# Performance work log

Hardware: AMD Instinct MI355X
Metric: run time of the kernel (lower is better)

Reference implementation:

```python
import jax, jax.numpy as jnp
import numpy as np

S = 64   # feature-map height/width = sqrt(qvk_dim)
M = 2    # memory_block_size


def _block_divide(t):
    # (b, c, S*S) -> (b, c, (S/M)**2, M*M), matching
    # Rearrange('b c (h m1) (w m2) -> b c (h w) (m1 m2)')
    b, c, _ = t.shape
    h = S // M
    t = t.reshape(b, c, h, M, h, M)
    t = jnp.transpose(t, (0, 1, 2, 4, 3, 5))
    return t.reshape(b, c, h * h, M * M)


def setup_inputs() -> dict:
    key = jax.random.key(0)
    k1, k2, k3, k4 = jax.random.split(key, 4)
    B, C, F = 64, 64, S * S
    x = jax.random.normal(k1, (B, C, F), dtype=jnp.float32)
    scale = 1.0 / np.sqrt(F)
    Wq = jax.random.normal(k2, (F, F), dtype=jnp.float32) * scale
    Wk = jax.random.normal(k3, (F, F), dtype=jnp.float32) * scale
    Wv = jax.random.normal(k4, (F, F), dtype=jnp.float32) * scale
    return {"x": x, "Wq": Wq, "Wk": Wk, "Wv": Wv}


def reference(x, Wq, Wk, Wv):
    # Linear(in, out, bias=False): y = x @ W.T, W: (out, in)
    q = _block_divide(jnp.einsum('bcf,qf->bcq', x, Wq))  # (b,c,n,g)
    k = _block_divide(jnp.einsum('bcf,qf->bcq', x, Wk))  # (b,c,n,p)
    v = _block_divide(jnp.einsum('bcf,qf->bcq', x, Wv))  # (b,c,n,p)
    # score[b,c,n,g,p] = q[b,c,n,g] * k[b,c,n,p]; softmax over p (dim=4)
    score = q[..., :, None] * k[..., None, :]             # (b,c,n,g,p)
    att = jax.nn.softmax(score, axis=-1)
    # matmul(att (g,p), v (p,1)) -> (g,1), then flatten blocks
    out = jnp.einsum('bcngp,bcnp->bcng', att, v)          # (b,c,n,g)
    b, c, n, g = out.shape
    return out.reshape(b, c, n * g)
```

## Files before the change

kernel.cpp:

```cpp
#include <hip/hip_runtime.h>

#define F        4096
#define NE       ((size_t)F * F)

typedef __attribute__((ext_vector_type(8))) short bf16x8;
typedef __attribute__((ext_vector_type(4))) float f32x4;

typedef const void __attribute__((address_space(1)))* gas1p;
typedef void __attribute__((address_space(3)))*       as3p;

__device__ __forceinline__ void gload16(const void* g, void* l) {
    __builtin_amdgcn_global_load_lds((gas1p)g, (as3p)l, 16, 0, 0);
}

__device__ __forceinline__ unsigned short f2bf(float f) {
    union { float f; unsigned int u; } c; c.f = f;
    unsigned int u = c.u;
    u += 0x7fffu + ((u >> 16) & 1u);
    return (unsigned short)(u >> 16);
}
__device__ __forceinline__ float bf2f(unsigned short u) {
    union { unsigned int u; float f; } c; c.u = ((unsigned int)u) << 16;
    return c.f;
}

__global__ void cvt_all(const float* __restrict__ s0, const float* __restrict__ s1,
                        const float* __restrict__ s2, const float* __restrict__ s3,
                        unsigned short* __restrict__ d0, unsigned short* __restrict__ d1,
                        unsigned short* __restrict__ d2, unsigned short* __restrict__ d3,
                        int n4) {
    const float* src = (blockIdx.y == 0) ? s0 : (blockIdx.y == 1) ? s1
                      : (blockIdx.y == 2) ? s2 : s3;
    unsigned short* dst = (blockIdx.y == 0) ? d0 : (blockIdx.y == 1) ? d1
                         : (blockIdx.y == 2) ? d2 : d3;
    int idx    = blockIdx.x * blockDim.x + threadIdx.x;
    int stride = gridDim.x * blockDim.x;
    const float4* in4 = (const float4*)src;
    ushort4* out4 = (ushort4*)dst;
    for (int i = idx; i < n4; i += stride) {
        float4 v = in4[i];
        ushort4 o;
        o.x = f2bf(v.x); o.y = f2bf(v.y); o.z = f2bf(v.z); o.w = f2bf(v.w);
        out4[i] = o;
    }
}

__device__ __forceinline__ int qo_map(int o) {
    int nblk = o >> 2, g = o & 3;
    return (nblk >> 5) * 128 + (g >> 1) * 64 + (nblk & 31) * 2 + (g & 1);
}

#define MFMA16(a, b, c) __builtin_amdgcn_mfma_f32_16x16x32_bf16(a, b, c, 0, 0, 0)

#define GBM 256
#define GBN 256
#define GBK 32
#define NKT (F / GBK)
#define ELPS (GBM * GBK)

__launch_bounds__(512, 1)
__global__ void gemm_qkv(const unsigned short* __restrict__ Xb,
                         const unsigned short* __restrict__ Qw,
                         const unsigned short* __restrict__ Kw,
                         const unsigned short* __restrict__ Vw,
                         unsigned short* __restrict__ qkv) {
    __shared__ __align__(16) unsigned short Als[4][GBM][GBK];
    __shared__ __align__(16) unsigned short Bls[4][GBN][GBK];

    const int tid  = threadIdx.x;
    const int lane = tid & 63;
    const int wid  = tid >> 6;
    const int wm   = wid >> 2;
    const int wn   = wid & 3;

    const int bid = blockIdx.x;
    const int swz = (bid & 7) * 96 + (bid >> 3);
    const int mt  = swz & 15;
    const int nt  = swz >> 4;
    const int bm  = mt * GBM;
    const int bnG = nt * GBN;
    const int mat = bnG >> 12;
    const int bn  = bnG & 4095;
    const unsigned short* __restrict__ Wsel = (mat == 0) ? Qw : (mat == 1) ? Kw : Vw;

    const int sr_row = tid >> 2;
    const int sr_chn = (tid & 3) ^ ((tid >> 3) & 3);
    const unsigned short* aSrc0 = Xb + (size_t)(bm + sr_row) * F + sr_chn * 8;
    const unsigned short* aSrc1 = aSrc0 + (size_t)128 * F;
    const unsigned short* bSrc0 = Wsel + (size_t)qo_map(bn + sr_row) * F + sr_chn * 8;
    const unsigned short* bSrc1 = Wsel + (size_t)qo_map(bn + 128 + sr_row) * F + sr_chn * 8;

#define STAGE_A(s, tt) do {                                                     \
        gload16(aSrc0 + (size_t)(tt) * GBK, (void*)&Als[s][wid * 16][0]);       \
        gload16(aSrc1 + (size_t)(tt) * GBK, (void*)&Als[s][128 + wid * 16][0]); \
    } while (0)
#define STAGE_B(s, tt) do {                                                     \
        gload16(bSrc0 + (size_t)(tt) * GBK, (void*)&Bls[s][wid * 16][0]);       \
        gload16(bSrc1 + (size_t)(tt) * GBK, (void*)&Bls[s][128 + wid * 16][0]); \
    } while (0)

    const int fr  = lane & 15;
    const int fq  = lane >> 4;
    const int fq2 = fq ^ ((fr >> 1) & 3);
    const unsigned short* aRd = &Als[0][wm * 128 + fr][fq2 * 8];
    const unsigned short* bRd = &Bls[0][wn * 64 + fr][fq2 * 8];

    f32x4 acc[8][4];
#pragma unroll
    for (int m = 0; m < 8; ++m)
#pragma unroll
        for (int n = 0; n < 4; ++n)
            acc[m][n] = (f32x4){0.f, 0.f, 0.f, 0.f};

    STAGE_A(0, 0); STAGE_B(0, 0);
    STAGE_A(1, 1); STAGE_B(1, 1);
    STAGE_A(2, 2); STAGE_B(2, 2);
    asm volatile("s_waitcnt vmcnt(4)" ::: "memory");
    __builtin_amdgcn_s_barrier();
    __builtin_amdgcn_sched_barrier(0);

    bf16x8 af[8], bf[4];
#pragma unroll
    for (int m = 0; m < 8; ++m) af[m] = *(const bf16x8*)(aRd + m * 512);
#pragma unroll
    for (int n = 0; n < 4; ++n) bf[n] = *(const bf16x8*)(bRd + n * 512);

#pragma unroll 4
    for (int t = 0; t < NKT; ++t) {
        const int sn = (t + 1) & 3;
        const int ss = (t + 3) & 3;
        const int tt = (t + 3) & (NKT - 1);
        const unsigned short* aN = aRd + sn * ELPS;
        const unsigned short* bN = bRd + sn * ELPS;

        __builtin_amdgcn_s_setprio(1);
#pragma unroll
        for (int m = 0; m < 8; ++m) {
#pragma unroll
            for (int n = 0; n < 4; ++n)
                acc[m][n] = MFMA16(af[m], bf[n], acc[m][n]);
            af[m] = *(const bf16x8*)(aN + m * 512);
        }
#pragma unroll
        for (int n = 0; n < 4; ++n)
            bf[n] = *(const bf16x8*)(bN + n * 512);
        __builtin_amdgcn_s_setprio(0);

        STAGE_A(ss, tt);
        STAGE_B(ss, tt);
        __builtin_amdgcn_sched_barrier(0);
        asm volatile("s_waitcnt vmcnt(4)" ::: "memory");
        __builtin_amdgcn_sched_barrier(0);
        __builtin_amdgcn_s_barrier();
    }

    unsigned short* outB = qkv + (size_t)mat * NE;
#pragma unroll
    for (int m = 0; m < 8; ++m) {
#pragma unroll
        for (int n = 0; n < 4; ++n) {
#pragma unroll
            for (int r = 0; r < 4; ++r) {
                int row = bm + wm * 128 + m * 16 + fq * 4 + r;
                int col = bn + wn * 64 + n * 16 + fr;
                outB[(size_t)row * F + col] = f2bf(acc[m][n][r]);
            }
        }
    }
#undef STAGE_A
#undef STAGE_B
}

__global__ void attn_ep(const unsigned short* __restrict__ qkv,
                        float* __restrict__ out) {
    const size_t NB = NE / 4;
    const ushort4* q4 = (const ushort4*)qkv;
    const ushort4* k4 = q4 + NB;
    const ushort4* v4 = k4 + NB;
    float4* o4 = (float4*)out;
    size_t i      = (size_t)blockIdx.x * blockDim.x + threadIdx.x;
    size_t stride = (size_t)gridDim.x * blockDim.x;
    for (; i < NB; i += stride) {
        ushort4 qu = q4[i], ku = k4[i], vu = v4[i];
        float q0 = bf2f(qu.x), q1 = bf2f(qu.y), q2 = bf2f(qu.z), q3 = bf2f(qu.w);
        float k0 = bf2f(ku.x), k1 = bf2f(ku.y), k2 = bf2f(ku.z), k3 = bf2f(ku.w);
        float v0 = bf2f(vu.x), v1 = bf2f(vu.y), v2 = bf2f(vu.z), v3 = bf2f(vu.w);
        float4 res;
#pragma unroll
        for (int g = 0; g < 4; ++g) {
            float qg = (g == 0) ? q0 : (g == 1) ? q1 : (g == 2) ? q2 : q3;
            float s0 = qg * k0, s1 = qg * k1, s2 = qg * k2, s3 = qg * k3;
            float mx = fmaxf(fmaxf(s0, s1), fmaxf(s2, s3));
            float e0 = __expf(s0 - mx), e1 = __expf(s1 - mx);
            float e2 = __expf(s2 - mx), e3 = __expf(s3 - mx);
            float num = e0 * v0 + e1 * v1 + e2 * v2 + e3 * v3;
            float den = e0 + e1 + e2 + e3;
            float r = num / den;
            if (g == 0) res.x = r; else if (g == 1) res.y = r;
            else if (g == 2) res.z = r; else res.w = r;
        }
        o4[i] = res;
    }
}

#define BM       128
#define BN       128
#define BK       32
#define NTHREADS 512
#define KTILES   (F / BK)

__launch_bounds__(NTHREADS, 1)
__global__ void fused_qkv_attn(const unsigned short* __restrict__ Xb,
                               const unsigned short* __restrict__ Qw,
                               const unsigned short* __restrict__ Kw,
                               const unsigned short* __restrict__ Vw,
                               float* __restrict__ out) {
    __shared__ __align__(16) unsigned short Alds[BM][BK];
    __shared__ __align__(16) unsigned short Blds[3][BN][BK];

    const int tid  = threadIdx.x;
    const int lane = tid & 63;
    const int wid  = tid >> 6;
    const int wm   = wid >> 1;
    const int wn   = wid & 1;

    const int bm = blockIdx.y * BM;
    const int bn = blockIdx.x * BN;

    const int srow   = wid * 16 + (lane >> 2);
    const int kchunk = (lane & 3) ^ ((lane >> 3) & 3);
    const int scol   = kchunk * 8;

    const unsigned short* aG = Xb + (size_t)(bm + srow) * F + scol;
    const int o  = bn + srow;
    const int qo = qo_map(o);
    const unsigned short* qG = Qw + (size_t)qo * F + scol;
    const unsigned short* kG = Kw + (size_t)qo * F + scol;
    const unsigned short* vG = Vw + (size_t)qo * F + scol;

    unsigned short* aL = &Alds[wid * 16][0];
    unsigned short* qL = &Blds[0][wid * 16][0];
    unsigned short* kL = &Blds[1][wid * 16][0];
    unsigned short* vL = &Blds[2][wid * 16][0];

    const int fr  = lane & 15;
    const int fq  = lane >> 4;
    const int fq2 = fq ^ ((fr >> 1) & 3);

    const unsigned short* aP[2];
#pragma unroll
    for (int m = 0; m < 2; ++m)
        aP[m] = &Alds[wm * 32 + m * 16 + fr][fq2 * 8];
    const unsigned short* bP[4];
#pragma unroll
    for (int n = 0; n < 4; ++n)
        bP[n] = &Blds[0][wn * 64 + n * 16 + fr][fq2 * 8];

    f32x4 acc[3][2][4];
#pragma unroll
    for (int t = 0; t < 3; ++t)
#pragma unroll
        for (int m = 0; m < 2; ++m)
#pragma unroll
            for (int n = 0; n < 4; ++n)
                acc[t][m][n] = (f32x4){0.f, 0.f, 0.f, 0.f};

    for (int kt = 0; kt < KTILES; ++kt) {
        gload16(aG, aL);
        gload16(qG, qL);
        gload16(kG, kL);
        gload16(vG, vL);
        aG += BK; qG += BK; kG += BK; vG += BK;
        __syncthreads();

        bf16x8 afr[2];
#pragma unroll
        for (int m = 0; m < 2; ++m)
            afr[m] = *(const bf16x8*)aP[m];

#pragma unroll
        for (int t = 0; t < 3; ++t) {
#pragma unroll
            for (int n = 0; n < 4; ++n) {
                bf16x8 bfr = *(const bf16x8*)(bP[n] + t * (BN * BK));
#pragma unroll
                for (int m = 0; m < 2; ++m)
                    acc[t][m][n] = MFMA16(afr[m], bfr, acc[t][m][n]);
            }
        }
        __syncthreads();
    }

#pragma unroll
    for (int m = 0; m < 2; ++m) {
#pragma unroll
        for (int n = 0; n < 4; ++n) {
#pragma unroll
            for (int r = 0; r < 4; ++r) {
                float q  = acc[0][m][n][r];
                float k0 = acc[1][m][n][r];
                float v0 = acc[2][m][n][r];
                float k1 = __shfl_xor(k0, 1);
                float k2 = __shfl_xor(k0, 2);
                float k3 = __shfl_xor(k0, 3);
                float v1 = __shfl_xor(v0, 1);
                float v2 = __shfl_xor(v0, 2);
                float v3 = __shfl_xor(v0, 3);
                float s0 = q * k0, s1 = q * k1, s2 = q * k2, s3 = q * k3;
                float mx = fmaxf(fmaxf(s0, s1), fmaxf(s2, s3));
                float e0 = __expf(s0 - mx), e1 = __expf(s1 - mx);
                float e2 = __expf(s2 - mx), e3 = __expf(s3 - mx);
                float num = e0 * v0 + e1 * v1 + e2 * v2 + e3 * v3;
                float den = e0 + e1 + e2 + e3;
                int row = bm + wm * 32 + m * 16 + fq * 4 + r;
                int oc  = bn + wn * 64 + n * 16 + fr;
                out[(size_t)row * F + oc] = num / den;
            }
        }
    }
}

extern "C" void kernel_launch(void* const* d_in, const int* in_sizes, int n_in,
                              void* d_out, int out_size, void* d_ws, size_t ws_size,
                              hipStream_t stream) {
    const float* x  = (const float*)d_in[0];
    const float* Wq = (const float*)d_in[1];
    const float* Wk = (const float*)d_in[2];
    const float* Wv = (const float*)d_in[3];
    float* out = (float*)d_out;

    unsigned short* xb  = (unsigned short*)d_ws;
    unsigned short* wqb = xb  + NE;
    unsigned short* wkb = wqb + NE;
    unsigned short* wvb = wkb + NE;
    unsigned short* qkv = wvb + NE;

    const int n4 = (int)(NE / 4);
    cvt_all<<<dim3(2048, 4), 256, 0, stream>>>(x, Wq, Wk, Wv, xb, wqb, wkb, wvb, n4);

    const size_t need_fast = NE * 2 * 7;
    if (ws_size >= need_fast) {
        gemm_qkv<<<768, 512, 0, stream>>>(xb, wqb, wkb, wvb, qkv);
        attn_ep<<<4096, 256, 0, stream>>>(qkv, out);
    } else {
        dim3 grid(F / BN, F / BM);
        fused_qkv_attn<<<grid, NTHREADS, 0, stream>>>(xb, wqb, wkb, wvb, out);
    }
}
```

Baseline: 465.9 us.

## Restructure QKV GEMM into 4-phase ping-pong pipeline with BK=64 double buffering

```diff
diff --git a/kernel.cpp b/kernel.cpp
--- a/kernel.cpp
+++ b/kernel.cpp
@@ -52,20 +52,18 @@
 
 #define MFMA16(a, b, c) __builtin_amdgcn_mfma_f32_16x16x32_bf16(a, b, c, 0, 0, 0)
 
-#define GBM 256
-#define GBN 256
-#define GBK 32
-#define NKT (F / GBK)
-#define ELPS (GBM * GBK)
-
-__launch_bounds__(512, 1)
+#define GBK  64
+#define NKT  (F / GBK)
+#define HTEL 8192
+
+__launch_bounds__(512, 2)
 __global__ void gemm_qkv(const unsigned short* __restrict__ Xb,
                          const unsigned short* __restrict__ Qw,
                          const unsigned short* __restrict__ Kw,
                          const unsigned short* __restrict__ Vw,
                          unsigned short* __restrict__ qkv) {
-    __shared__ __align__(16) unsigned short Als[4][GBM][GBK];
-    __shared__ __align__(16) unsigned short Bls[4][GBN][GBK];
+    __shared__ __align__(16) unsigned short Als[2][2][HTEL];
+    __shared__ __align__(16) unsigned short Bls[2][2][HTEL];
 
     const int tid  = threadIdx.x;
     const int lane = tid & 63;
@@ -77,33 +75,72 @@
     const int swz = (bid & 7) * 96 + (bid >> 3);
     const int mt  = swz & 15;
     const int nt  = swz >> 4;
-    const int bm  = mt * GBM;
-    const int bnG = nt * GBN;
+    const int bm  = mt * 256;
+    const int bnG = nt * 256;
     const int mat = bnG >> 12;
     const int bn  = bnG & 4095;
     const unsigned short* __restrict__ Wsel = (mat == 0) ? Qw : (mat == 1) ? Kw : Vw;
 
-    const int sr_row = tid >> 2;
-    const int sr_chn = (tid & 3) ^ ((tid >> 3) & 3);
-    const unsigned short* aSrc0 = Xb + (size_t)(bm + sr_row) * F + sr_chn * 8;
-    const unsigned short* aSrc1 = aSrc0 + (size_t)128 * F;
-    const unsigned short* bSrc0 = Wsel + (size_t)qo_map(bn + sr_row) * F + sr_chn * 8;
-    const unsigned short* bSrc1 = Wsel + (size_t)qo_map(bn + 128 + sr_row) * F + sr_chn * 8;
-
-#define STAGE_A(s, tt) do {                                                     \
-        gload16(aSrc0 + (size_t)(tt) * GBK, (void*)&Als[s][wid * 16][0]);       \
-        gload16(aSrc1 + (size_t)(tt) * GBK, (void*)&Als[s][128 + wid * 16][0]); \
+    const int trow  = tid >> 3;
+    const int tslot = (tid & 7) ^ (trow & 7);
+    const unsigned short* aP[2][2];
+    const unsigned short* bP[2][2];
+#pragma unroll
+    for (int h = 0; h < 2; ++h)
+#pragma unroll
+        for (int r = 0; r < 2; ++r) {
+            aP[h][r] = Xb   + (size_t)(bm + h * 128 + r * 64 + trow) * F + tslot * 8;
+            bP[h][r] = Wsel + (size_t)qo_map(bn + h * 128 + r * 64 + trow) * F + tslot * 8;
+        }
+#define STAGE_A(buf, h, tt) do {                                               \
+        gload16(aP[h][0] + (size_t)(tt) * GBK, (void*)&Als[buf][h][wid * 512]);        \
+        gload16(aP[h][1] + (size_t)(tt) * GBK, (void*)&Als[buf][h][4096 + wid * 512]); \
     } while (0)
-#define STAGE_B(s, tt) do {                                                     \
-        gload16(bSrc0 + (size_t)(tt) * GBK, (void*)&Bls[s][wid * 16][0]);       \
-        gload16(bSrc1 + (size_t)(tt) * GBK, (void*)&Bls[s][128 + wid * 16][0]); \
+#define STAGE_B(buf, h, tt) do {                                               \
+        gload16(bP[h][0] + (size_t)(tt) * GBK, (void*)&Bls[buf][h][wid * 512]);        \
+        gload16(bP[h][1] + (size_t)(tt) * GBK, (void*)&Bls[buf][h][4096 + wid * 512]); \
     } while (0)
 
-    const int fr  = lane & 15;
-    const int fq  = lane >> 4;
-    const int fq2 = fq ^ ((fr >> 1) & 3);
-    const unsigned short* aRd = &Als[0][wm * 128 + fr][fq2 * 8];
-    const unsigned short* bRd = &Bls[0][wn * 64 + fr][fq2 * 8];
+    const int fr   = lane & 15;
+    const int fq   = lane >> 4;
+    const int flo  = fr & 7;
+    const int bh   = wn >> 1;
+    const int bcol = (wn & 1) * 64;
+    const int sw0  = ((0 * 4 + fq) ^ flo) * 8;
+    const int sw1  = ((1 * 4 + fq) ^ flo) * 8;
+
+#define READ_A(buf, mh, AF) do {                                                \
+        _Pragma("unroll")                                                       \
+        for (int i = 0; i < 4; ++i) {                                           \
+            const unsigned short* p = &Als[buf][wm][((mh) * 64 + i * 16 + fr) * 64]; \
+            AF[i * 2 + 0] = *(const bf16x8*)(p + sw0);                          \
+            AF[i * 2 + 1] = *(const bf16x8*)(p + sw1);                          \
+        }                                                                       \
+    } while (0)
+#define READ_B(buf, nh, BF) do {                                                \
+        _Pragma("unroll")                                                       \
+        for (int j = 0; j < 2; ++j) {                                           \
+            const unsigned short* p = &Bls[buf][bh][(bcol + (nh) * 32 + j * 16 + fr) * 64]; \
+            BF[j * 2 + 0] = *(const bf16x8*)(p + sw0);                          \
+            BF[j * 2 + 1] = *(const bf16x8*)(p + sw1);                          \
+        }                                                                       \
+    } while (0)
+
+#define QMFMA(AF, BF, MB, NB) do {                                              \
+        _Pragma("unroll")                                                       \
+        for (int i = 0; i < 4; ++i)                                             \
+            _Pragma("unroll")                                                   \
+            for (int j = 0; j < 2; ++j) {                                       \
+                acc[(MB) + i][(NB) + j] =                                       \
+                    MFMA16(AF[i * 2], BF[j * 2], acc[(MB) + i][(NB) + j]);      \
+                acc[(MB) + i][(NB) + j] =                                       \
+                    MFMA16(AF[i * 2 + 1], BF[j * 2 + 1], acc[(MB) + i][(NB) + j]); \
+            }                                                                   \
+    } while (0)
+
+#define SBAR  __builtin_amdgcn_s_barrier()
+#define SCB   __builtin_amdgcn_sched_barrier(0)
+#define LGKM0 asm volatile("s_waitcnt lgkmcnt(0)" ::: "memory")
 
     f32x4 acc[8][4];
 #pragma unroll
@@ -112,47 +149,56 @@
         for (int n = 0; n < 4; ++n)
             acc[m][n] = (f32x4){0.f, 0.f, 0.f, 0.f};
 
-    STAGE_A(0, 0); STAGE_B(0, 0);
-    STAGE_A(1, 1); STAGE_B(1, 1);
-    STAGE_A(2, 2); STAGE_B(2, 2);
-    asm volatile("s_waitcnt vmcnt(4)" ::: "memory");
-    __builtin_amdgcn_s_barrier();
-    __builtin_amdgcn_sched_barrier(0);
-
-    bf16x8 af[8], bf[4];
-#pragma unroll
-    for (int m = 0; m < 8; ++m) af[m] = *(const bf16x8*)(aRd + m * 512);
-#pragma unroll
-    for (int n = 0; n < 4; ++n) bf[n] = *(const bf16x8*)(bRd + n * 512);
-
-#pragma unroll 4
+    STAGE_A(0, 0, 0); STAGE_A(0, 1, 0); STAGE_B(0, 0, 0); STAGE_B(0, 1, 0);
+    STAGE_A(1, 0, 1); STAGE_A(1, 1, 1); STAGE_B(1, 0, 1); STAGE_B(1, 1, 1);
+    asm volatile("s_waitcnt vmcnt(8)" ::: "memory");
+    SBAR; SCB;
+
+    bf16x8 aF[8], bF0[4], bF1[4];
+
+#pragma unroll 2
     for (int t = 0; t < NKT; ++t) {
-        const int sn = (t + 1) & 3;
-        const int ss = (t + 3) & 3;
-        const int tt = (t + 3) & (NKT - 1);
-        const unsigned short* aN = aRd + sn * ELPS;
-        const unsigned short* bN = bRd + sn * ELPS;
-
+        const int b  = t & 1;
+        const int t2 = (t + 2) & (NKT - 1);
+
+        READ_A(b, 0, aF);
+        READ_B(b, 0, bF0);
+        SCB; SBAR;
+        LGKM0; SCB;
         __builtin_amdgcn_s_setprio(1);
-#pragma unroll
-        for (int m = 0; m < 8; ++m) {
-#pragma unroll
-            for (int n = 0; n < 4; ++n)
-                acc[m][n] = MFMA16(af[m], bf[n], acc[m][n]);
-            af[m] = *(const bf16x8*)(aN + m * 512);
-        }
-#pragma unroll
-        for (int n = 0; n < 4; ++n)
-            bf[n] = *(const bf16x8*)(bN + n * 512);
+        QMFMA(aF, bF0, 0, 0);
         __builtin_amdgcn_s_setprio(0);
-
-        STAGE_A(ss, tt);
-        STAGE_B(ss, tt);
-        __builtin_amdgcn_sched_barrier(0);
-        asm volatile("s_waitcnt vmcnt(4)" ::: "memory");
-        __builtin_amdgcn_sched_barrier(0);
-        __builtin_amdgcn_s_barrier();
-    }
+        SCB; SBAR; SCB;
+
+        READ_B(b, 1, bF1);
+        SCB; SBAR;
+        LGKM0; SCB;
+        __builtin_amdgcn_s_setprio(1);
+        QMFMA(aF, bF1, 0, 2);
+        __builtin_amdgcn_s_setprio(0);
+        SCB; SBAR; SCB;
+
+        READ_A(b, 1, aF);
+        STAGE_B(b, 0, t2);
+        STAGE_B(b, 1, t2);
+        SCB; SBAR;
+        LGKM0; SCB;
+        __builtin_amdgcn_s_setprio(1);
+        QMFMA(aF, bF1, 4, 2);
+        __builtin_amdgcn_s_setprio(0);
+        SCB; SBAR; SCB;
+
+        STAGE_A(b, 0, t2);
+        STAGE_A(b, 1, t2);
+        SCB; SBAR;
+        __builtin_amdgcn_s_setprio(1);
+        QMFMA(aF, bF0, 4, 0);
+        __builtin_amdgcn_s_setprio(0);
+        asm volatile("s_waitcnt vmcnt(8)" ::: "memory");
+        SCB; SBAR; SCB;
+    }
+
+    asm volatile("s_waitcnt vmcnt(0)" ::: "memory");
 
     unsigned short* outB = qkv + (size_t)mat * NE;
 #pragma unroll
@@ -169,6 +215,12 @@
     }
 #undef STAGE_A
 #undef STAGE_B
+#undef READ_A
+#undef READ_B
+#undef QMFMA
+#undef SBAR
+#undef SCB
+#undef LGKM0
 }
 
 __global__ void attn_ep(const unsigned short* __restrict__ qkv,
```

Measured after the change: 478.5 us. 2.7% more time.

## Switch QKV GEMM inner loop from 16x16x32 to 32x32x16 bf16 MFMA tiles

Applied to the files above, without the earlier changes.

```diff
diff --git a/kernel.cpp b/kernel.cpp
--- a/kernel.cpp
+++ b/kernel.cpp
@@ -3,8 +3,9 @@
 #define F        4096
 #define NE       ((size_t)F * F)
 
-typedef __attribute__((ext_vector_type(8))) short bf16x8;
-typedef __attribute__((ext_vector_type(4))) float f32x4;
+typedef __attribute__((ext_vector_type(8)))  short bf16x8;
+typedef __attribute__((ext_vector_type(4)))  float f32x4;
+typedef __attribute__((ext_vector_type(16))) float f32x16;
 
 typedef const void __attribute__((address_space(1)))* gas1p;
 typedef void __attribute__((address_space(3)))*       as3p;
@@ -51,6 +52,7 @@
 }
 
 #define MFMA16(a, b, c) __builtin_amdgcn_mfma_f32_16x16x32_bf16(a, b, c, 0, 0, 0)
+#define MFMA32(a, b, c) __builtin_amdgcn_mfma_f32_32x32x16_bf16(a, b, c, 0, 0, 0)
 
 #define GBM 256
 #define GBN 256
@@ -99,18 +101,29 @@
         gload16(bSrc1 + (size_t)(tt) * GBK, (void*)&Bls[s][128 + wid * 16][0]); \
     } while (0)
 
-    const int fr  = lane & 15;
-    const int fq  = lane >> 4;
-    const int fq2 = fq ^ ((fr >> 1) & 3);
-    const unsigned short* aRd = &Als[0][wm * 128 + fr][fq2 * 8];
-    const unsigned short* bRd = &Bls[0][wn * 64 + fr][fq2 * 8];
-
-    f32x4 acc[8][4];
-#pragma unroll
-    for (int m = 0; m < 8; ++m)
-#pragma unroll
-        for (int n = 0; n < 4; ++n)
-            acc[m][n] = (f32x4){0.f, 0.f, 0.f, 0.f};
+    const int lrow = lane & 31;
+    const int l5   = lane >> 5;
+    const int rx   = (lrow >> 1) & 3;
+    const int se0  = ((0 * 2 + l5) ^ rx) * 8;
+    const int se1  = ((1 * 2 + l5) ^ rx) * 8;
+
+    const unsigned short* aRow[4];
+#pragma unroll
+    for (int mi = 0; mi < 4; ++mi)
+        aRow[mi] = &Als[0][wm * 128 + mi * 32 + lrow][0];
+    const unsigned short* bRow[2];
+#pragma unroll
+    for (int nj = 0; nj < 2; ++nj)
+        bRow[nj] = &Bls[0][wn * 64 + nj * 32 + lrow][0];
+
+    f32x16 acc[4][2];
+#pragma unroll
+    for (int mi = 0; mi < 4; ++mi)
+#pragma unroll
+        for (int nj = 0; nj < 2; ++nj)
+#pragma unroll
+            for (int r = 0; r < 16; ++r)
+                acc[mi][nj][r] = 0.f;
 
     STAGE_A(0, 0); STAGE_B(0, 0);
     STAGE_A(1, 1); STAGE_B(1, 1);
@@ -119,31 +132,42 @@
     __builtin_amdgcn_s_barrier();
     __builtin_amdgcn_sched_barrier(0);
 
-    bf16x8 af[8], bf[4];
-#pragma unroll
-    for (int m = 0; m < 8; ++m) af[m] = *(const bf16x8*)(aRd + m * 512);
-#pragma unroll
-    for (int n = 0; n < 4; ++n) bf[n] = *(const bf16x8*)(bRd + n * 512);
-
-#pragma unroll 4
+    bf16x8 af0[4], af1[4], bf0[2], bf1[2];
+#pragma unroll
+    for (int mi = 0; mi < 4; ++mi) {
+        af0[mi] = *(const bf16x8*)(aRow[mi] + se0);
+        af1[mi] = *(const bf16x8*)(aRow[mi] + se1);
+    }
+#pragma unroll
+    for (int nj = 0; nj < 2; ++nj) {
+        bf0[nj] = *(const bf16x8*)(bRow[nj] + se0);
+        bf1[nj] = *(const bf16x8*)(bRow[nj] + se1);
+    }
+
+#pragma unroll 2
     for (int t = 0; t < NKT; ++t) {
         const int sn = (t + 1) & 3;
         const int ss = (t + 3) & 3;
         const int tt = (t + 3) & (NKT - 1);
-        const unsigned short* aN = aRd + sn * ELPS;
-        const unsigned short* bN = bRd + sn * ELPS;
+        const int so = sn * ELPS;
 
         __builtin_amdgcn_s_setprio(1);
 #pragma unroll
-        for (int m = 0; m < 8; ++m) {
-#pragma unroll
-            for (int n = 0; n < 4; ++n)
-                acc[m][n] = MFMA16(af[m], bf[n], acc[m][n]);
-            af[m] = *(const bf16x8*)(aN + m * 512);
-        }
-#pragma unroll
-        for (int n = 0; n < 4; ++n)
-            bf[n] = *(const bf16x8*)(bN + n * 512);
+        for (int mi = 0; mi < 4; ++mi) {
+            acc[mi][0] = MFMA32(af0[mi], bf0[0], acc[mi][0]);
+            acc[mi][1] = MFMA32(af0[mi], bf0[1], acc[mi][1]);
+            af0[mi] = *(const bf16x8*)(aRow[mi] + so + se0);
+        }
+        bf0[0] = *(const bf16x8*)(bRow[0] + so + se0);
+        bf0[1] = *(const bf16x8*)(bRow[1] + so + se0);
+#pragma unroll
+        for (int mi = 0; mi < 4; ++mi) {
+            acc[mi][0] = MFMA32(af1[mi], bf1[0], acc[mi][0]);
+            acc[mi][1] = MFMA32(af1[mi], bf1[1], acc[mi][1]);
+            af1[mi] = *(const bf16x8*)(aRow[mi] + so + se1);
+        }
+        bf1[0] = *(const bf16x8*)(bRow[0] + so + se1);
+        bf1[1] = *(const bf16x8*)(bRow[1] + so + se1);
         __builtin_amdgcn_s_setprio(0);
 
         STAGE_A(ss, tt);
@@ -154,16 +178,18 @@
         __builtin_amdgcn_s_barrier();
     }
 
+    asm volatile("s_waitcnt vmcnt(0)" ::: "memory");
+
     unsigned short* outB = qkv + (size_t)mat * NE;
 #pragma unroll
-    for (int m = 0; m < 8; ++m) {
-#pragma unroll
-        for (int n = 0; n < 4; ++n) {
-#pragma unroll
-            for (int r = 0; r < 4; ++r) {
-                int row = bm + wm * 128 + m * 16 + fq * 4 + r;
-                int col = bn + wn * 64 + n * 16 + fr;
-                outB[(size_t)row * F + col] = f2bf(acc[m][n][r]);
+    for (int mi = 0; mi < 4; ++mi) {
+#pragma unroll
+        for (int nj = 0; nj < 2; ++nj) {
+#pragma unroll
+            for (int r = 0; r < 16; ++r) {
+                int row = bm + wm * 128 + mi * 32 + (r & 3) + 8 * (r >> 2) + 4 * l5;
+                int col = bn + wn * 64 + nj * 32 + lrow;
+                outB[(size_t)row * F + col] = f2bf(acc[mi][nj][r]);
             }
         }
     }
```

Measured after the change: 472.3 us. About the same (+1.4%).

## Retile QKV GEMM to 128x256 blocks with 4 waves, 2 blocks/CU, 3-stage pipeline

Applied to the files above, without the earlier changes.

```diff
diff --git a/kernel.cpp b/kernel.cpp
--- a/kernel.cpp
+++ b/kernel.cpp
@@ -3,8 +3,8 @@
 #define F        4096
 #define NE       ((size_t)F * F)
 
-typedef __attribute__((ext_vector_type(8))) short bf16x8;
-typedef __attribute__((ext_vector_type(4))) float f32x4;
+typedef __attribute__((ext_vector_type(8)))  short bf16x8;
+typedef __attribute__((ext_vector_type(4)))  float f32x4;
 
 typedef const void __attribute__((address_space(1)))* gas1p;
 typedef void __attribute__((address_space(3)))*       as3p;
@@ -52,123 +52,152 @@
 
 #define MFMA16(a, b, c) __builtin_amdgcn_mfma_f32_16x16x32_bf16(a, b, c, 0, 0, 0)
 
-#define GBM 256
+#define GBM 128
 #define GBN 256
 #define GBK 32
 #define NKT (F / GBK)
-#define ELPS (GBM * GBK)
-
-__launch_bounds__(512, 1)
+#define AELPS (GBM * GBK)
+#define BELPS (GBN * GBK)
+
+__launch_bounds__(256, 2)
 __global__ void gemm_qkv(const unsigned short* __restrict__ Xb,
                          const unsigned short* __restrict__ Qw,
                          const unsigned short* __restrict__ Kw,
                          const unsigned short* __restrict__ Vw,
                          unsigned short* __restrict__ qkv) {
-    __shared__ __align__(16) unsigned short Als[4][GBM][GBK];
-    __shared__ __align__(16) unsigned short Bls[4][GBN][GBK];
+    __shared__ __align__(16) unsigned short Als[3][GBM][GBK];
+    __shared__ __align__(16) unsigned short Bls[3][GBN][GBK];
 
     const int tid  = threadIdx.x;
     const int lane = tid & 63;
     const int wid  = tid >> 6;
-    const int wm   = wid >> 2;
-    const int wn   = wid & 3;
+    const int wwm  = wid >> 1;
+    const int wwn  = wid & 1;
 
     const int bid = blockIdx.x;
-    const int swz = (bid & 7) * 96 + (bid >> 3);
-    const int mt  = swz & 15;
-    const int nt  = swz >> 4;
+    const int swz = (bid & 7) * 192 + (bid >> 3);
+    const int mt  = swz & 31;
+    const int nt  = swz >> 5;
     const int bm  = mt * GBM;
     const int bnG = nt * GBN;
     const int mat = bnG >> 12;
     const int bn  = bnG & 4095;
     const unsigned short* __restrict__ Wsel = (mat == 0) ? Qw : (mat == 1) ? Kw : Vw;
 
-    const int sr_row = tid >> 2;
-    const int sr_chn = (tid & 3) ^ ((tid >> 3) & 3);
-    const unsigned short* aSrc0 = Xb + (size_t)(bm + sr_row) * F + sr_chn * 8;
-    const unsigned short* aSrc1 = aSrc0 + (size_t)128 * F;
-    const unsigned short* bSrc0 = Wsel + (size_t)qo_map(bn + sr_row) * F + sr_chn * 8;
-    const unsigned short* bSrc1 = Wsel + (size_t)qo_map(bn + 128 + sr_row) * F + sr_chn * 8;
-
-#define STAGE_A(s, tt) do {                                                     \
-        gload16(aSrc0 + (size_t)(tt) * GBK, (void*)&Als[s][wid * 16][0]);       \
-        gload16(aSrc1 + (size_t)(tt) * GBK, (void*)&Als[s][128 + wid * 16][0]); \
-    } while (0)
-#define STAGE_B(s, tt) do {                                                     \
-        gload16(bSrc0 + (size_t)(tt) * GBK, (void*)&Bls[s][wid * 16][0]);       \
-        gload16(bSrc1 + (size_t)(tt) * GBK, (void*)&Bls[s][128 + wid * 16][0]); \
+    const int rloc = tid >> 2;
+    const int chn  = (tid & 3) ^ ((tid >> 3) & 3);
+    const unsigned short* aSrc0 = Xb + (size_t)(bm + rloc) * F + chn * 8;
+    const unsigned short* aSrc1 = aSrc0 + (size_t)64 * F;
+    const unsigned short* bSrcR[4];
+#pragma unroll
+    for (int q = 0; q < 4; ++q)
+        bSrcR[q] = Wsel + (size_t)qo_map(bn + q * 64 + rloc) * F + chn * 8;
+
+#define STAGE(s, tt) do {                                                         \
+        gload16(aSrc0    + (size_t)(tt) * GBK, (void*)&Als[s][wid * 16][0]);      \
+        gload16(aSrc1    + (size_t)(tt) * GBK, (void*)&Als[s][64 + wid * 16][0]); \
+        gload16(bSrcR[0] + (size_t)(tt) * GBK, (void*)&Bls[s][wid * 16][0]);      \
+        gload16(bSrcR[1] + (size_t)(tt) * GBK, (void*)&Bls[s][64 + wid * 16][0]); \
+        gload16(bSrcR[2] + (size_t)(tt) * GBK, (void*)&Bls[s][128 + wid * 16][0]);\
+        gload16(bSrcR[3] + (size_t)(tt) * GBK, (void*)&Bls[s][192 + wid * 16][0]);\
     } while (0)
 
     const int fr  = lane & 15;
     const int fq  = lane >> 4;
     const int fq2 = fq ^ ((fr >> 1) & 3);
-    const unsigned short* aRd = &Als[0][wm * 128 + fr][fq2 * 8];
-    const unsigned short* bRd = &Bls[0][wn * 64 + fr][fq2 * 8];
-
-    f32x4 acc[8][4];
-#pragma unroll
-    for (int m = 0; m < 8; ++m)
-#pragma unroll
-        for (int n = 0; n < 4; ++n)
-            acc[m][n] = (f32x4){0.f, 0.f, 0.f, 0.f};
-
-    STAGE_A(0, 0); STAGE_B(0, 0);
-    STAGE_A(1, 1); STAGE_B(1, 1);
-    STAGE_A(2, 2); STAGE_B(2, 2);
-    asm volatile("s_waitcnt vmcnt(4)" ::: "memory");
+    const unsigned short* aRd = &Als[0][wwm * 64 + fr][fq2 * 8];
+    const unsigned short* bRd = &Bls[0][wwn * 128 + fr][fq2 * 8];
+
+    f32x4 acc[4][8];
+#pragma unroll
+    for (int mi = 0; mi < 4; ++mi)
+#pragma unroll
+        for (int nj = 0; nj < 8; ++nj)
+            acc[mi][nj] = (f32x4){0.f, 0.f, 0.f, 0.f};
+
+    STAGE(0, 0);
+    STAGE(1, 1);
+    asm volatile("s_waitcnt vmcnt(6)" ::: "memory");
     __builtin_amdgcn_s_barrier();
-    __builtin_amdgcn_sched_barrier(0);
-
-    bf16x8 af[8], bf[4];
-#pragma unroll
-    for (int m = 0; m < 8; ++m) af[m] = *(const bf16x8*)(aRd + m * 512);
-#pragma unroll
-    for (int n = 0; n < 4; ++n) bf[n] = *(const bf16x8*)(bRd + n * 512);
-
-#pragma unroll 4
-    for (int t = 0; t < NKT; ++t) {
-        const int sn = (t + 1) & 3;
-        const int ss = (t + 3) & 3;
-        const int tt = (t + 3) & (NKT - 1);
-        const unsigned short* aN = aRd + sn * ELPS;
-        const unsigned short* bN = bRd + sn * ELPS;
-
-        __builtin_amdgcn_s_setprio(1);
-#pragma unroll
-        for (int m = 0; m < 8; ++m) {
-#pragma unroll
-            for (int n = 0; n < 4; ++n)
-                acc[m][n] = MFMA16(af[m], bf[n], acc[m][n]);
-            af[m] = *(const bf16x8*)(aN + m * 512);
-        }
-#pragma unroll
-        for (int n = 0; n < 4; ++n)
-            bf[n] = *(const bf16x8*)(bN + n * 512);
-        __builtin_amdgcn_s_setprio(0);
-
-        STAGE_A(ss, tt);
-        STAGE_B(ss, tt);
-        __builtin_amdgcn_sched_barrier(0);
-        asm volatile("s_waitcnt vmcnt(4)" ::: "memory");
-        __builtin_amdgcn_sched_barrier(0);
-        __builtin_amdgcn_s_barrier();
+
+#define MQ(nj, BF) do {                                                           \
+        _Pragma("unroll")                                                         \
+        for (int mi = 0; mi < 4; ++mi)                                            \
+            acc[mi][nj] = MFMA16(af[mi], BF, acc[mi][nj]);                        \
+    } while (0)
+
+#define ITER(t, cur, stg, STG) do {                                               \
+        const unsigned short* aC = aRd + (cur) * AELPS;                           \
+        const unsigned short* bC = bRd + (cur) * BELPS;                           \
+        bf16x8 af[4];                                                             \
+        _Pragma("unroll")                                                         \
+        for (int mi = 0; mi < 4; ++mi)                                            \
+            af[mi] = *(const bf16x8*)(aC + mi * 512);                             \
+        bf16x8 b0 = *(const bf16x8*)(bC + 0 * 512);                               \
+        bf16x8 b1 = *(const bf16x8*)(bC + 1 * 512);                               \
+        __builtin_amdgcn_s_setprio(1);                                            \
+        MQ(0, b0);  b0 = *(const bf16x8*)(bC + 2 * 512);                          \
+        MQ(1, b1);  b1 = *(const bf16x8*)(bC + 3 * 512);                          \
+        MQ(2, b0);  b0 = *(const bf16x8*)(bC + 4 * 512);                          \
+        MQ(3, b1);  b1 = *(const bf16x8*)(bC + 5 * 512);                          \
+        MQ(4, b0);  b0 = *(const bf16x8*)(bC + 6 * 512);                          \
+        MQ(5, b1);  b1 = *(const bf16x8*)(bC + 7 * 512);                          \
+        MQ(6, b0);                                                                \
+        MQ(7, b1);                                                                \
+        __builtin_amdgcn_s_setprio(0);                                            \
+        if (STG) {                                                                \
+            STAGE(stg, (t) + 2);                                                  \
+            __builtin_amdgcn_sched_barrier(0);                                    \
+            asm volatile("s_waitcnt vmcnt(6)" ::: "memory");                      \
+        } else {                                                                  \
+            __builtin_amdgcn_sched_barrier(0);                                    \
+            asm volatile("s_waitcnt vmcnt(0)" ::: "memory");                      \
+        }                                                                         \
+        __builtin_amdgcn_sched_barrier(0);                                        \
+        __builtin_amdgcn_s_barrier();                                             \
+    } while (0)
+
+    for (int t = 0; t < 126; t += 3) {
+        ITER(t,     0, 2, true);
+        ITER(t + 1, 1, 0, true);
+        ITER(t + 2, 2, 1, true);
+    }
+    ITER(126, 0, 2, false);
+    {
+        const unsigned short* aC = aRd + 1 * AELPS;
+        const unsigned short* bC = bRd + 1 * BELPS;
+        bf16x8 af[4];
+#pragma unroll
+        for (int mi = 0; mi < 4; ++mi)
+            af[mi] = *(const bf16x8*)(aC + mi * 512);
+        bf16x8 b0 = *(const bf16x8*)(bC + 0 * 512);
+        bf16x8 b1 = *(const bf16x8*)(bC + 1 * 512);
+        MQ(0, b0);  b0 = *(const bf16x8*)(bC + 2 * 512);
+        MQ(1, b1);  b1 = *(const bf16x8*)(bC + 3 * 512);
+        MQ(2, b0);  b0 = *(const bf16x8*)(bC + 4 * 512);
+        MQ(3, b1);  b1 = *(const bf16x8*)(bC + 5 * 512);
+        MQ(4, b0);  b0 = *(const bf16x8*)(bC + 6 * 512);
+        MQ(5, b1);  b1 = *(const bf16x8*)(bC + 7 * 512);
+        MQ(6, b0);
+        MQ(7, b1);
     }
 
     unsigned short* outB = qkv + (size_t)mat * NE;
 #pragma unroll
-    for (int m = 0; m < 8; ++m) {
-#pragma unroll
-        for (int n = 0; n < 4; ++n) {
+    for (int mi = 0; mi < 4; ++mi) {
+#pragma unroll
+        for (int nj = 0; nj < 8; ++nj) {
 #pragma unroll
             for (int r = 0; r < 4; ++r) {
-                int row = bm + wm * 128 + m * 16 + fq * 4 + r;
-                int col = bn + wn * 64 + n * 16 + fr;
-                outB[(size_t)row * F + col] = f2bf(acc[m][n][r]);
+                int row = bm + wwm * 64 + mi * 16 + fq * 4 + r;
+                int col = bn + wwn * 128 + nj * 16 + fr;
+                outB[(size_t)row * F + col] = f2bf(acc[mi][nj][r]);
             }
         }
     }
-#undef STAGE_A
-#undef STAGE_B
+#undef ITER
+#undef MQ
+#undef STAGE
 }
 
 __global__ void attn_ep(const unsigned short* __restrict__ qkv,
@@ -340,7 +369,7 @@
 
     const size_t need_fast = NE * 2 * 7;
     if (ws_size >= need_fast) {
-        gemm_qkv<<<768, 512, 0, stream>>>(xb, wqb, wkb, wvb, qkv);
+        gemm_qkv<<<1536, 256, 0, stream>>>(xb, wqb, wkb, wvb, qkv);
         attn_ep<<<4096, 256, 0, stream>>>(qkv, out);
     } else {
         dim3 grid(F / BN, F / BM);
```

New measurement: 518.2 us. +11.2%, slower.
